# Kernel tuning notes

Hardware: AMD Instinct MI355X
Metric: run time of the kernel (lower is better)

Reference implementation:

```python
import jax, jax.numpy as jnp
import numpy as np
import math

B, C, L = 16, 2048, 64

def setup_inputs() -> dict:
    key = jax.random.key(0)
    kq, kk, kv = jax.random.split(key, 3)
    q = jax.random.normal(kq, (B, C, L), dtype=jnp.float32)
    k = jax.random.normal(kk, (B, C, L), dtype=jnp.float32)
    v = jax.random.normal(kv, (B, C, L), dtype=jnp.float32)
    return {"q": q, "k": k, "v": v}

def reference(q, k, v):
    b, c, l = q.shape
    # Faithful to the torch source: k is RESHAPED (row-major), not transposed.
    k_t = k.reshape(b, l, c)                      # (b, l, c)
    score = jnp.matmul(q, k_t) / math.sqrt(l)     # (b, c, c)
    # nn.Softmax() with no dim on a 3D tensor -> torch implicit dim = 0 (batch axis)
    score = jax.nn.softmax(score, axis=0)
    return jnp.matmul(score, v)                   # (b, c, l)
```

## Files before the change

### kernel.cpp

```cpp
#include <hip/hip_runtime.h>

typedef __attribute__((ext_vector_type(8))) short short8;
typedef __attribute__((ext_vector_type(4))) float float4v;

#define BATCH 16
#define CDIM 2048
#define LDIM 64
#define BSTRIDE (CDIM * LDIM)

__device__ __forceinline__ float bf2f(unsigned short u) {
    return __uint_as_float(((unsigned int)u) << 16);
}
__device__ __forceinline__ unsigned short f2bf(float f) {
    unsigned int x = __float_as_uint(f);
    x += 0x7fffu + ((x >> 16) & 1u);
    return (unsigned short)(x >> 16);
}
__device__ __forceinline__ void dma16(const void* g, void* l) {
    __builtin_amdgcn_global_load_lds(
        (const __attribute__((address_space(1))) void*)g,
        (__attribute__((address_space(3))) void*)l, 16, 0, 0);
}

__global__ __launch_bounds__(256) void prepass_kernel(
    const float* __restrict__ q, const float* __restrict__ k, const float* __restrict__ v,
    unsigned short* __restrict__ qb,
    unsigned short* __restrict__ kT, unsigned short* __restrict__ vS)
{
    __shared__ unsigned short T[64][68];
    const int bx = blockIdx.x;
    const int t = threadIdx.x;

    if (bx < 1024) {
        int i = bx * 256 + t;
        const float4v* src = (const float4v*)q + (size_t)i * 2;
        float4v x0 = src[0], x1 = src[1];
        unsigned int u0 = f2bf(x0[0] * 0.125f) | ((unsigned)f2bf(x0[1] * 0.125f) << 16);
        unsigned int u1 = f2bf(x0[2] * 0.125f) | ((unsigned)f2bf(x0[3] * 0.125f) << 16);
        unsigned int u2 = f2bf(x1[0] * 0.125f) | ((unsigned)f2bf(x1[1] * 0.125f) << 16);
        unsigned int u3 = f2bf(x1[2] * 0.125f) | ((unsigned)f2bf(x1[3] * 0.125f) << 16);
        int b = i >> 14, r = i & 16383, m = r >> 3, j = r & 7;
        *(uint4*)(qb + (size_t)b * BSTRIDE + m * 64 + (j ^ (m & 7)) * 8) =
            make_uint4(u0, u1, u2, u3);
    } else if (bx < 1536) {
        int idx = bx - 1024, b = idx >> 5, n0 = (idx & 31) * 64;
        const float* src = k + (size_t)b * BSTRIDE + (size_t)(t >> 2) * 2048 + n0 + (t & 3) * 16;
#pragma unroll
        for (int kk = 0; kk < 4; kk++) {
            float4v x = *(const float4v*)(src + kk * 4);
#pragma unroll
            for (int e = 0; e < 4; e++)
                T[t >> 2][(t & 3) * 16 + kk * 4 + e] = f2bf(x[e]);
        }
        __syncthreads();
        unsigned short* dst = kT + (size_t)b * BSTRIDE;
        int n = t & 63;
#pragma unroll
        for (int jj = 0; jj < 2; jj++) {
            int j = (t >> 6) * 2 + jj;
            ushort4 g0, g1;
#pragma unroll
            for (int e = 0; e < 4; e++) { g0[e] = T[j * 8 + e][n]; g1[e] = T[j * 8 + 4 + e][n]; }
            *(uint4*)(dst + (size_t)(n0 + n) * 64 + (j ^ (n & 7)) * 8) =
                make_uint4(g0.x | ((unsigned)g0.y << 16), g0.z | ((unsigned)g0.w << 16),
                           g1.x | ((unsigned)g1.y << 16), g1.z | ((unsigned)g1.w << 16));
        }
    } else {
        int idx = bx - 1536, b = idx >> 5, n0 = (idx & 31) * 64;
        const float* src = v + (size_t)b * BSTRIDE + (size_t)n0 * 64 +
                           (size_t)(t >> 2) * 64 + (t & 3) * 16;
#pragma unroll
        for (int kk = 0; kk < 4; kk++) {
            float4v x = *(const float4v*)(src + kk * 4);
#pragma unroll
            for (int e = 0; e < 4; e++)
                T[t >> 2][(t & 3) * 16 + kk * 4 + e] = f2bf(x[e]);
        }
        __syncthreads();
        unsigned short* dst = vS + (size_t)b * BSTRIDE;
        int j = t & 63, qc = t >> 6;
#pragma unroll
        for (int nb = 0; nb < 2; nb++) {
            ushort4 g0, g1;
#pragma unroll
            for (int e = 0; e < 4; e++) {
                g0[e] = T[nb * 32 + qc * 8 + e][j];
                g1[e] = T[nb * 32 + qc * 8 + 4 + e][j];
            }
            *(uint4*)(dst + (size_t)(n0 / 32 + nb) * 2048 + j * 32 + (qc ^ (j & 3)) * 8) =
                make_uint4(g0.x | ((unsigned)g0.y << 16), g0.z | ((unsigned)g0.w << 16),
                           g1.x | ((unsigned)g1.y << 16), g1.z | ((unsigned)g1.w << 16));
        }
    }
}

__global__ __launch_bounds__(256, 2) void dinv_kernel(
    const unsigned short* __restrict__ qb, const unsigned short* __restrict__ kT,
    unsigned short* __restrict__ Dt)
{
    __shared__ unsigned short Sq[2][8192];
    __shared__ unsigned short Sk[2][4096];
    const int tid = threadIdx.x, w = tid >> 6, lane = tid & 63;
    const int c = lane & 15, q = lane >> 4;
    const int mt = blockIdx.x & 15, ng = blockIdx.x >> 4;
    const int m0 = mt * 128, n0 = ng * 64;

    float4v Dacc[2][4];
#pragma unroll
    for (int ms = 0; ms < 2; ms++)
#pragma unroll
        for (int nt = 0; nt < 4; nt++) Dacc[ms][nt] = (float4v){0.f, 0.f, 0.f, 0.f};

    {
        const char* qg = (const char*)(qb + (size_t)m0 * 64);
        const char* kg = (const char*)(kT + (size_t)n0 * 64);
#pragma unroll
        for (int kk = 0; kk < 4; kk++)
            dma16(qg + (w * 4 + kk) * 1024 + lane * 16, (char*)Sq[0] + (w * 4 + kk) * 1024);
        dma16(kg + (w * 2 + 0) * 1024 + lane * 16, (char*)Sk[0] + (w * 2 + 0) * 1024);
        dma16(kg + (w * 2 + 1) * 1024 + lane * 16, (char*)Sk[0] + (w * 2 + 1) * 1024);
    }

    for (int bb = 0; bb < BATCH; bb++) {
        const int p = bb & 1;
        if (bb < BATCH - 1) {
            const char* qg = (const char*)(qb + (size_t)(bb + 1) * BSTRIDE + (size_t)m0 * 64);
            const char* kg = (const char*)(kT + (size_t)(bb + 1) * BSTRIDE + (size_t)n0 * 64);
#pragma unroll
            for (int kk = 0; kk < 4; kk++)
                dma16(qg + (w * 4 + kk) * 1024 + lane * 16, (char*)Sq[p ^ 1] + (w * 4 + kk) * 1024);
            dma16(kg + (w * 2 + 0) * 1024 + lane * 16, (char*)Sk[p ^ 1] + (w * 2 + 0) * 1024);
            dma16(kg + (w * 2 + 1) * 1024 + lane * 16, (char*)Sk[p ^ 1] + (w * 2 + 1) * 1024);
            asm volatile("s_waitcnt vmcnt(6)" ::: "memory");
        } else {
            asm volatile("s_waitcnt vmcnt(0)" ::: "memory");
        }
        asm volatile("s_barrier" ::: "memory");

        short8 Qf[2][2];
#pragma unroll
        for (int ms = 0; ms < 2; ms++)
#pragma unroll
            for (int h = 0; h < 2; h++)
                Qf[ms][h] = *(const short8*)&Sq[p][(w * 32 + ms * 16 + c) * 64 +
                                                  ((h * 4 + q) ^ (c & 7)) * 8];
#pragma unroll
        for (int nt = 0; nt < 4; nt++) {
            short8 A0 = *(const short8*)&Sk[p][(nt * 16 + c) * 64 + (q ^ (c & 7)) * 8];
            short8 A1 = *(const short8*)&Sk[p][(nt * 16 + c) * 64 + ((4 + q) ^ (c & 7)) * 8];
#pragma unroll
            for (int ms = 0; ms < 2; ms++) {
                float4v d = (float4v){0.f, 0.f, 0.f, 0.f};
                d = __builtin_amdgcn_mfma_f32_16x16x32_bf16(A0, Qf[ms][0], d, 0, 0, 0);
                d = __builtin_amdgcn_mfma_f32_16x16x32_bf16(A1, Qf[ms][1], d, 0, 0, 0);
#pragma unroll
                for (int r = 0; r < 4; r++) Dacc[ms][nt][r] += __expf(d[r]);
            }
        }
        asm volatile("s_barrier" ::: "memory");
    }

#pragma unroll
    for (int ms = 0; ms < 2; ms++)
#pragma unroll
        for (int nt = 0; nt < 4; nt++) {
            unsigned int x = f2bf(1.f / Dacc[ms][nt][0]) |
                             ((unsigned)f2bf(1.f / Dacc[ms][nt][1]) << 16);
            unsigned int y = f2bf(1.f / Dacc[ms][nt][2]) |
                             ((unsigned)f2bf(1.f / Dacc[ms][nt][3]) << 16);
            size_t T = (size_t)(mt * 64 + ng * 2 + (nt >> 1));
            *(uint2*)((char*)Dt + T * 8192 + w * 2048 + (ms * 2 + (nt & 1)) * 512 + lane * 8) =
                make_uint2(x, y);
        }
}

__global__ __launch_bounds__(1024, 4) void attn_main_kernel(
    const unsigned short* __restrict__ qb, const unsigned short* __restrict__ kT,
    const unsigned short* __restrict__ vS, const unsigned short* __restrict__ Dt,
    float* __restrict__ out)
{
    __shared__ unsigned short Sk[4][2][2048];
    __shared__ unsigned short Sv[4][2][2048];
    __shared__ unsigned short Ep[16][2][16][40];

    const int tid = threadIdx.x, w = tid >> 6, lane = tid & 63;
    const int c = lane & 15, q = lane >> 4;
    const int g = w >> 2, ns = w & 3;
    const int b = blockIdx.x & 15, mt = blockIdx.x >> 4;
    const int m0 = mt * 128 + g * 32;
    const int nbase = ns * 512;

    const unsigned short* qb_b = qb + (size_t)b * BSTRIDE;
    const char* kbase = (const char*)(kT + (size_t)b * BSTRIDE);
    const char* vbase = (const char*)(vS + (size_t)b * BSTRIDE);

    short8 Qf[2][2];
#pragma unroll
    for (int ms = 0; ms < 2; ms++)
#pragma unroll
        for (int h = 0; h < 2; h++)
            Qf[ms][h] = *(const short8*)(qb_b + (m0 + ms * 16 + c) * 64 +
                                         ((h * 4 + q) ^ (c & 7)) * 8);
    float4v acc[2][4];
#pragma unroll
    for (int ms = 0; ms < 2; ms++)
#pragma unroll
        for (int jt = 0; jt < 4; jt++) acc[ms][jt] = (float4v){0.f, 0.f, 0.f, 0.f};

    dma16(kbase + (size_t)nbase * 128 + g * 1024 + lane * 16, (char*)Sk[ns][0] + g * 1024);
    dma16(vbase + (size_t)(ns * 16) * 4096 + g * 1024 + lane * 16, (char*)Sv[ns][0] + g * 1024);

    for (int st = 0; st < 16; st++) {
        const int p = st & 1;
        if (st < 15) {
            const int n1 = nbase + (st + 1) * 32;
            dma16(kbase + (size_t)n1 * 128 + g * 1024 + lane * 16, (char*)Sk[ns][p ^ 1] + g * 1024);
            dma16(vbase + (size_t)(ns * 16 + st + 1) * 4096 + g * 1024 + lane * 16,
                  (char*)Sv[ns][p ^ 1] + g * 1024);
            asm volatile("s_waitcnt vmcnt(2)" ::: "memory");
        } else {
            asm volatile("s_waitcnt vmcnt(0)" ::: "memory");
        }
        asm volatile("s_barrier" ::: "memory");

        const char* dtb = (const char*)Dt + (size_t)(mt * 64 + ns * 16 + st) * 8192 +
                          g * 2048 + lane * 8;
        uint2 du[2][2];
        du[0][0] = *(const uint2*)(dtb + 0);
        du[0][1] = *(const uint2*)(dtb + 512);
        du[1][0] = *(const uint2*)(dtb + 1024);
        du[1][1] = *(const uint2*)(dtb + 1536);

#pragma unroll
        for (int nt = 0; nt < 2; nt++) {
            short8 A0 = *(const short8*)&Sk[ns][p][(nt * 16 + c) * 64 + (q ^ (c & 7)) * 8];
            short8 A1 = *(const short8*)&Sk[ns][p][(nt * 16 + c) * 64 + ((4 + q) ^ (c & 7)) * 8];
#pragma unroll
            for (int ms = 0; ms < 2; ms++) {
                float4v d = (float4v){0.f, 0.f, 0.f, 0.f};
                d = __builtin_amdgcn_mfma_f32_16x16x32_bf16(A0, Qf[ms][0], d, 0, 0, 0);
                d = __builtin_amdgcn_mfma_f32_16x16x32_bf16(A1, Qf[ms][1], d, 0, 0, 0);
                uint2 u2 = du[ms][nt];
                ushort4 e;
                e.x = f2bf(__expf(d[0]) * __uint_as_float(u2.x << 16));
                e.y = f2bf(__expf(d[1]) * __uint_as_float(u2.x & 0xffff0000u));
                e.z = f2bf(__expf(d[2]) * __uint_as_float(u2.y << 16));
                e.w = f2bf(__expf(d[3]) * __uint_as_float(u2.y & 0xffff0000u));
                *(ushort4*)&Ep[w][ms][c][nt * 16 + q * 4] = e;
            }
        }
        asm volatile("s_waitcnt lgkmcnt(0)" ::: "memory");

        short8 Vf[4];
#pragma unroll
        for (int jt = 0; jt < 4; jt++)
            Vf[jt] = *(const short8*)&Sv[ns][p][(jt * 16 + c) * 32 + (q ^ (c & 3)) * 8];
#pragma unroll
        for (int ms = 0; ms < 2; ms++) {
            short8 Pf = *(const short8*)&Ep[w][ms][c][q * 8];
#pragma unroll
            for (int jt = 0; jt < 4; jt++)
                acc[ms][jt] = __builtin_amdgcn_mfma_f32_16x16x32_bf16(Pf, Vf[jt], acc[ms][jt], 0, 0, 0);
        }
        asm volatile("s_barrier" ::: "memory");
    }

    float* Racc = (float*)&Sk[0][0][0];
    float* Rg = Racc + g * 2176;
    __syncthreads();
#pragma unroll 1
    for (int round = 0; round < 4; round++) {
        if (ns == round) {
#pragma unroll
            for (int ms = 0; ms < 2; ms++)
#pragma unroll
                for (int jt = 0; jt < 4; jt++)
#pragma unroll
                    for (int r = 0; r < 4; r++) {
                        int idx = (ms * 16 + q * 4 + r) * 68 + jt * 16 + c;
                        if (round == 0) Rg[idx] = acc[ms][jt][r];
                        else Rg[idx] += acc[ms][jt][r];
                    }
        }
        __syncthreads();
    }
    {
        int mrow = tid >> 3, col0 = (tid & 7) * 8;
        const float* src = Racc + (mrow >> 5) * 2176 + (mrow & 31) * 68 + col0;
        float4v v0 = *(const float4v*)(src);
        float4v v1 = *(const float4v*)(src + 4);
        float* dst = out + ((size_t)b * CDIM + mt * 128 + mrow) * LDIM + col0;
        *(float4v*)(dst) = v0;
        *(float4v*)(dst + 4) = v1;
    }
}

extern "C" void kernel_launch(void* const* d_in, const int* in_sizes, int n_in,
                              void* d_out, int out_size, void* d_ws, size_t ws_size,
                              hipStream_t stream) {
    const float* q = (const float*)d_in[0];
    const float* k = (const float*)d_in[1];
    const float* v = (const float*)d_in[2];
    float* out = (float*)d_out;

    unsigned short* qb = (unsigned short*)d_ws;
    unsigned short* kT = qb + (size_t)BATCH * BSTRIDE;
    unsigned short* vS = kT + (size_t)BATCH * BSTRIDE;
    unsigned short* Dt = vS + (size_t)BATCH * BSTRIDE;

    prepass_kernel<<<2048, 256, 0, stream>>>(q, k, v, qb, kT, vS);
    dinv_kernel<<<512, 256, 0, stream>>>(qb, kT, Dt);
    attn_main_kernel<<<256, 1024, 0, stream>>>(qb, kT, vS, Dt, out);
}
```

Before: 129.6 us.

## Use exp2 with folded scale, register-shuffle P, smaller main blocks, new Dt layout

Folds log2(e) into the q pre-scale so the kernels can call the hardware exp2 builtin, and uses the rcp builtin for the denominators. The main kernel moves from 1024-thread to 512-thread blocks over 64-row tiles. It builds the P operand with lane shuffles instead of an LDS round trip, prefetches the denominator tiles one step ahead in a coalesced layout, and replaces the four-round reduction with a two-stage one. The dinv kernel gets a flat shared buffer, a higher occupancy hint and a single wait-and-barrier per iteration. This adds a matching swizzle change in V and risks more register pressure and shuffle cost.

```diff
diff --git a/kernel.cpp b/kernel.cpp
--- a/kernel.cpp
+++ b/kernel.cpp
@@ -7,6 +7,14 @@
 #define CDIM 2048
 #define LDIM 64
 #define BSTRIDE (CDIM * LDIM)
+
+#if __has_builtin(__builtin_amdgcn_exp2f)
+#define EXPW(x) __builtin_amdgcn_exp2f(x)
+#define QSCALE 0.18033688011112042f
+#else
+#define EXPW(x) __expf(x)
+#define QSCALE 0.125f
+#endif
 
 __device__ __forceinline__ float bf2f(unsigned short u) {
     return __uint_as_float(((unsigned int)u) << 16);
@@ -35,10 +43,10 @@
         int i = bx * 256 + t;
         const float4v* src = (const float4v*)q + (size_t)i * 2;
         float4v x0 = src[0], x1 = src[1];
-        unsigned int u0 = f2bf(x0[0] * 0.125f) | ((unsigned)f2bf(x0[1] * 0.125f) << 16);
-        unsigned int u1 = f2bf(x0[2] * 0.125f) | ((unsigned)f2bf(x0[3] * 0.125f) << 16);
-        unsigned int u2 = f2bf(x1[0] * 0.125f) | ((unsigned)f2bf(x1[1] * 0.125f) << 16);
-        unsigned int u3 = f2bf(x1[2] * 0.125f) | ((unsigned)f2bf(x1[3] * 0.125f) << 16);
+        unsigned int u0 = f2bf(x0[0] * QSCALE) | ((unsigned)f2bf(x0[1] * QSCALE) << 16);
+        unsigned int u1 = f2bf(x0[2] * QSCALE) | ((unsigned)f2bf(x0[3] * QSCALE) << 16);
+        unsigned int u2 = f2bf(x1[0] * QSCALE) | ((unsigned)f2bf(x1[1] * QSCALE) << 16);
+        unsigned int u3 = f2bf(x1[2] * QSCALE) | ((unsigned)f2bf(x1[3] * QSCALE) << 16);
         int b = i >> 14, r = i & 16383, m = r >> 3, j = r & 7;
         *(uint4*)(qb + (size_t)b * BSTRIDE + m * 64 + (j ^ (m & 7)) * 8) =
             make_uint4(u0, u1, u2, u3);
@@ -79,6 +87,7 @@
         __syncthreads();
         unsigned short* dst = vS + (size_t)b * BSTRIDE;
         int j = t & 63, qc = t >> 6;
+        int sw = qc ^ (j & 3) ^ ((j >> 2) & 3);
 #pragma unroll
         for (int nb = 0; nb < 2; nb++) {
             ushort4 g0, g1;
@@ -87,23 +96,23 @@
                 g0[e] = T[nb * 32 + qc * 8 + e][j];
                 g1[e] = T[nb * 32 + qc * 8 + 4 + e][j];
             }
-            *(uint4*)(dst + (size_t)(n0 / 32 + nb) * 2048 + j * 32 + (qc ^ (j & 3)) * 8) =
+            *(uint4*)(dst + (size_t)(n0 / 32 + nb) * 2048 + j * 32 + sw * 8) =
                 make_uint4(g0.x | ((unsigned)g0.y << 16), g0.z | ((unsigned)g0.w << 16),
                            g1.x | ((unsigned)g1.y << 16), g1.z | ((unsigned)g1.w << 16));
         }
     }
 }
 
-__global__ __launch_bounds__(256, 2) void dinv_kernel(
+__global__ __launch_bounds__(256, 3) void dinv_kernel(
     const unsigned short* __restrict__ qb, const unsigned short* __restrict__ kT,
     unsigned short* __restrict__ Dt)
 {
-    __shared__ unsigned short Sq[2][8192];
-    __shared__ unsigned short Sk[2][4096];
+    __shared__ __align__(16) unsigned char smem[49152];
+
     const int tid = threadIdx.x, w = tid >> 6, lane = tid & 63;
     const int c = lane & 15, q = lane >> 4;
-    const int mt = blockIdx.x & 15, ng = blockIdx.x >> 4;
-    const int m0 = mt * 128, n0 = ng * 64;
+    const int mtB = blockIdx.x & 15, ng = blockIdx.x >> 4;
+    const int m0 = mtB * 128, n0 = ng * 64;
 
     float4v Dacc[2][4];
 #pragma unroll
@@ -116,90 +125,92 @@
         const char* kg = (const char*)(kT + (size_t)n0 * 64);
 #pragma unroll
         for (int kk = 0; kk < 4; kk++)
-            dma16(qg + (w * 4 + kk) * 1024 + lane * 16, (char*)Sq[0] + (w * 4 + kk) * 1024);
-        dma16(kg + (w * 2 + 0) * 1024 + lane * 16, (char*)Sk[0] + (w * 2 + 0) * 1024);
-        dma16(kg + (w * 2 + 1) * 1024 + lane * 16, (char*)Sk[0] + (w * 2 + 1) * 1024);
+            dma16(qg + (w * 4 + kk) * 1024 + lane * 16, (char*)smem + (w * 4 + kk) * 1024);
+        dma16(kg + (w * 2 + 0) * 1024 + lane * 16, (char*)smem + 32768 + (w * 2 + 0) * 1024);
+        dma16(kg + (w * 2 + 1) * 1024 + lane * 16, (char*)smem + 32768 + (w * 2 + 1) * 1024);
     }
 
     for (int bb = 0; bb < BATCH; bb++) {
         const int p = bb & 1;
+        asm volatile("s_waitcnt vmcnt(0)" ::: "memory");
+        asm volatile("s_barrier" ::: "memory");
         if (bb < BATCH - 1) {
             const char* qg = (const char*)(qb + (size_t)(bb + 1) * BSTRIDE + (size_t)m0 * 64);
             const char* kg = (const char*)(kT + (size_t)(bb + 1) * BSTRIDE + (size_t)n0 * 64);
 #pragma unroll
             for (int kk = 0; kk < 4; kk++)
-                dma16(qg + (w * 4 + kk) * 1024 + lane * 16, (char*)Sq[p ^ 1] + (w * 4 + kk) * 1024);
-            dma16(kg + (w * 2 + 0) * 1024 + lane * 16, (char*)Sk[p ^ 1] + (w * 2 + 0) * 1024);
-            dma16(kg + (w * 2 + 1) * 1024 + lane * 16, (char*)Sk[p ^ 1] + (w * 2 + 1) * 1024);
-            asm volatile("s_waitcnt vmcnt(6)" ::: "memory");
-        } else {
-            asm volatile("s_waitcnt vmcnt(0)" ::: "memory");
-        }
-        asm volatile("s_barrier" ::: "memory");
-
+                dma16(qg + (w * 4 + kk) * 1024 + lane * 16,
+                      (char*)smem + (p ^ 1) * 16384 + (w * 4 + kk) * 1024);
+            dma16(kg + (w * 2 + 0) * 1024 + lane * 16,
+                  (char*)smem + 32768 + (p ^ 1) * 8192 + (w * 2 + 0) * 1024);
+            dma16(kg + (w * 2 + 1) * 1024 + lane * 16,
+                  (char*)smem + 32768 + (p ^ 1) * 8192 + (w * 2 + 1) * 1024);
+        }
+        const char* sq = (const char*)smem + p * 16384;
+        const char* sk = (const char*)smem + 32768 + p * 8192;
         short8 Qf[2][2];
 #pragma unroll
         for (int ms = 0; ms < 2; ms++)
 #pragma unroll
             for (int h = 0; h < 2; h++)
-                Qf[ms][h] = *(const short8*)&Sq[p][(w * 32 + ms * 16 + c) * 64 +
-                                                  ((h * 4 + q) ^ (c & 7)) * 8];
+                Qf[ms][h] = *(const short8*)(sq + (w * 32 + ms * 16 + c) * 128 +
+                                             ((h * 4 + q) ^ (c & 7)) * 16);
 #pragma unroll
         for (int nt = 0; nt < 4; nt++) {
-            short8 A0 = *(const short8*)&Sk[p][(nt * 16 + c) * 64 + (q ^ (c & 7)) * 8];
-            short8 A1 = *(const short8*)&Sk[p][(nt * 16 + c) * 64 + ((4 + q) ^ (c & 7)) * 8];
+            short8 A0 = *(const short8*)(sk + (nt * 16 + c) * 128 + ((q) ^ (c & 7)) * 16);
+            short8 A1 = *(const short8*)(sk + (nt * 16 + c) * 128 + ((4 + q) ^ (c & 7)) * 16);
 #pragma unroll
             for (int ms = 0; ms < 2; ms++) {
                 float4v d = (float4v){0.f, 0.f, 0.f, 0.f};
                 d = __builtin_amdgcn_mfma_f32_16x16x32_bf16(A0, Qf[ms][0], d, 0, 0, 0);
                 d = __builtin_amdgcn_mfma_f32_16x16x32_bf16(A1, Qf[ms][1], d, 0, 0, 0);
 #pragma unroll
-                for (int r = 0; r < 4; r++) Dacc[ms][nt][r] += __expf(d[r]);
+                for (int r = 0; r < 4; r++) Dacc[ms][nt][r] += EXPW(d[r]);
             }
         }
-        asm volatile("s_barrier" ::: "memory");
     }
 
 #pragma unroll
     for (int ms = 0; ms < 2; ms++)
 #pragma unroll
         for (int nt = 0; nt < 4; nt++) {
-            unsigned int x = f2bf(1.f / Dacc[ms][nt][0]) |
-                             ((unsigned)f2bf(1.f / Dacc[ms][nt][1]) << 16);
-            unsigned int y = f2bf(1.f / Dacc[ms][nt][2]) |
-                             ((unsigned)f2bf(1.f / Dacc[ms][nt][3]) << 16);
-            size_t T = (size_t)(mt * 64 + ng * 2 + (nt >> 1));
-            *(uint2*)((char*)Dt + T * 8192 + w * 2048 + (ms * 2 + (nt & 1)) * 512 + lane * 8) =
+            unsigned int x = f2bf(__builtin_amdgcn_rcpf(Dacc[ms][nt][0])) |
+                             ((unsigned)f2bf(__builtin_amdgcn_rcpf(Dacc[ms][nt][1])) << 16);
+            unsigned int y = f2bf(__builtin_amdgcn_rcpf(Dacc[ms][nt][2])) |
+                             ((unsigned)f2bf(__builtin_amdgcn_rcpf(Dacc[ms][nt][3])) << 16);
+            size_t tm = (size_t)(mtB * 8 + w * 2 + ms);
+            size_t tp = (size_t)(ng * 2 + (nt >> 1));
+            *(uint2*)((char*)Dt + (tm * 64 + tp) * 1024 + c * 64 + q * 16 + (nt & 1) * 8) =
                 make_uint2(x, y);
         }
 }
 
-__global__ __launch_bounds__(1024, 4) void attn_main_kernel(
+__global__ __launch_bounds__(512, 4) void attn_main_kernel(
     const unsigned short* __restrict__ qb, const unsigned short* __restrict__ kT,
     const unsigned short* __restrict__ vS, const unsigned short* __restrict__ Dt,
     float* __restrict__ out)
 {
-    __shared__ unsigned short Sk[4][2][2048];
-    __shared__ unsigned short Sv[4][2][2048];
-    __shared__ unsigned short Ep[16][2][16][40];
+    __shared__ __align__(16) unsigned char smem[65536];
 
     const int tid = threadIdx.x, w = tid >> 6, lane = tid & 63;
     const int c = lane & 15, q = lane >> 4;
     const int g = w >> 2, ns = w & 3;
     const int b = blockIdx.x & 15, mt = blockIdx.x >> 4;
-    const int m0 = mt * 128 + g * 32;
+    const int m0 = mt * 64;
     const int nbase = ns * 512;
 
     const unsigned short* qb_b = qb + (size_t)b * BSTRIDE;
     const char* kbase = (const char*)(kT + (size_t)b * BSTRIDE);
     const char* vbase = (const char*)(vS + (size_t)b * BSTRIDE);
+    char* skb = (char*)smem + ns * 8192;
+    char* svb = (char*)smem + 32768 + ns * 8192;
 
     short8 Qf[2][2];
 #pragma unroll
     for (int ms = 0; ms < 2; ms++)
 #pragma unroll
         for (int h = 0; h < 2; h++)
-            Qf[ms][h] = *(const short8*)(qb_b + (m0 + ms * 16 + c) * 64 +
+            Qf[ms][h] = *(const short8*)(qb_b + (m0 + g * 32 + ms * 16 + c) * 64 +
                                          ((h * 4 + q) ^ (c & 7)) * 8);
     float4v acc[2][4];
 #pragma unroll
@@ -207,91 +218,120 @@
 #pragma unroll
         for (int jt = 0; jt < 4; jt++) acc[ms][jt] = (float4v){0.f, 0.f, 0.f, 0.f};
 
-    dma16(kbase + (size_t)nbase * 128 + g * 1024 + lane * 16, (char*)Sk[ns][0] + g * 1024);
-    dma16(vbase + (size_t)(ns * 16) * 4096 + g * 1024 + lane * 16, (char*)Sv[ns][0] + g * 1024);
+    const char* dtw0 = (const char*)Dt +
+        ((size_t)(mt * 4 + g * 2 + 0) * 64 + ns * 16) * 1024 + c * 64 + q * 16;
+    const char* dtw1 = dtw0 + (size_t)64 * 1024;
+
+    dma16(kbase + (size_t)nbase * 128 + (2 * g + 0) * 1024 + lane * 16, skb + (2 * g + 0) * 1024);
+    dma16(kbase + (size_t)nbase * 128 + (2 * g + 1) * 1024 + lane * 16, skb + (2 * g + 1) * 1024);
+    dma16(vbase + (size_t)(ns * 16) * 4096 + (2 * g + 0) * 1024 + lane * 16, svb + (2 * g + 0) * 1024);
+    dma16(vbase + (size_t)(ns * 16) * 4096 + (2 * g + 1) * 1024 + lane * 16, svb + (2 * g + 1) * 1024);
+    uint4 du[2];
+    du[0] = *(const uint4*)(dtw0);
+    du[1] = *(const uint4*)(dtw1);
 
     for (int st = 0; st < 16; st++) {
         const int p = st & 1;
+        asm volatile("s_waitcnt vmcnt(0)" ::: "memory");
+        asm volatile("s_barrier" ::: "memory");
+
+        uint4 nu[2] = {du[0], du[1]};
         if (st < 15) {
             const int n1 = nbase + (st + 1) * 32;
-            dma16(kbase + (size_t)n1 * 128 + g * 1024 + lane * 16, (char*)Sk[ns][p ^ 1] + g * 1024);
-            dma16(vbase + (size_t)(ns * 16 + st + 1) * 4096 + g * 1024 + lane * 16,
-                  (char*)Sv[ns][p ^ 1] + g * 1024);
-            asm volatile("s_waitcnt vmcnt(2)" ::: "memory");
-        } else {
-            asm volatile("s_waitcnt vmcnt(0)" ::: "memory");
-        }
-        asm volatile("s_barrier" ::: "memory");
-
-        const char* dtb = (const char*)Dt + (size_t)(mt * 64 + ns * 16 + st) * 8192 +
-                          g * 2048 + lane * 8;
-        uint2 du[2][2];
-        du[0][0] = *(const uint2*)(dtb + 0);
-        du[0][1] = *(const uint2*)(dtb + 512);
-        du[1][0] = *(const uint2*)(dtb + 1024);
-        du[1][1] = *(const uint2*)(dtb + 1536);
-
+            dma16(kbase + (size_t)n1 * 128 + (2 * g + 0) * 1024 + lane * 16,
+                  skb + (p ^ 1) * 4096 + (2 * g + 0) * 1024);
+            dma16(kbase + (size_t)n1 * 128 + (2 * g + 1) * 1024 + lane * 16,
+                  skb + (p ^ 1) * 4096 + (2 * g + 1) * 1024);
+            dma16(vbase + (size_t)(ns * 16 + st + 1) * 4096 + (2 * g + 0) * 1024 + lane * 16,
+                  svb + (p ^ 1) * 4096 + (2 * g + 0) * 1024);
+            dma16(vbase + (size_t)(ns * 16 + st + 1) * 4096 + (2 * g + 1) * 1024 + lane * 16,
+                  svb + (p ^ 1) * 4096 + (2 * g + 1) * 1024);
+            nu[0] = *(const uint4*)(dtw0 + (size_t)(st + 1) * 1024);
+            nu[1] = *(const uint4*)(dtw1 + (size_t)(st + 1) * 1024);
+        }
+
+        const char* skp = skb + p * 4096;
+        unsigned int pr[2][2][2];
 #pragma unroll
         for (int nt = 0; nt < 2; nt++) {
-            short8 A0 = *(const short8*)&Sk[ns][p][(nt * 16 + c) * 64 + (q ^ (c & 7)) * 8];
-            short8 A1 = *(const short8*)&Sk[ns][p][(nt * 16 + c) * 64 + ((4 + q) ^ (c & 7)) * 8];
+            short8 A0 = *(const short8*)(skp + (nt * 16 + c) * 128 + ((q) ^ (c & 7)) * 16);
+            short8 A1 = *(const short8*)(skp + (nt * 16 + c) * 128 + ((4 + q) ^ (c & 7)) * 16);
 #pragma unroll
             for (int ms = 0; ms < 2; ms++) {
                 float4v d = (float4v){0.f, 0.f, 0.f, 0.f};
                 d = __builtin_amdgcn_mfma_f32_16x16x32_bf16(A0, Qf[ms][0], d, 0, 0, 0);
                 d = __builtin_amdgcn_mfma_f32_16x16x32_bf16(A1, Qf[ms][1], d, 0, 0, 0);
-                uint2 u2 = du[ms][nt];
-                ushort4 e;
-                e.x = f2bf(__expf(d[0]) * __uint_as_float(u2.x << 16));
-                e.y = f2bf(__expf(d[1]) * __uint_as_float(u2.x & 0xffff0000u));
-                e.z = f2bf(__expf(d[2]) * __uint_as_float(u2.y << 16));
-                e.w = f2bf(__expf(d[3]) * __uint_as_float(u2.y & 0xffff0000u));
-                *(ushort4*)&Ep[w][ms][c][nt * 16 + q * 4] = e;
+                unsigned int ux = nt ? du[ms].z : du[ms].x;
+                unsigned int uy = nt ? du[ms].w : du[ms].y;
+                float p0 = EXPW(d[0]) * __uint_as_float(ux << 16);
+                float p1 = EXPW(d[1]) * __uint_as_float(ux & 0xffff0000u);
+                float p2 = EXPW(d[2]) * __uint_as_float(uy << 16);
+                float p3 = EXPW(d[3]) * __uint_as_float(uy & 0xffff0000u);
+                pr[ms][nt][0] = f2bf(p0) | ((unsigned)f2bf(p1) << 16);
+                pr[ms][nt][1] = f2bf(p2) | ((unsigned)f2bf(p3) << 16);
             }
         }
-        asm volatile("s_waitcnt lgkmcnt(0)" ::: "memory");
-
-        short8 Vf[4];
-#pragma unroll
-        for (int jt = 0; jt < 4; jt++)
-            Vf[jt] = *(const short8*)&Sv[ns][p][(jt * 16 + c) * 32 + (q ^ (c & 3)) * 8];
-#pragma unroll
-        for (int ms = 0; ms < 2; ms++) {
-            short8 Pf = *(const short8*)&Ep[w][ms][c][q * 8];
-#pragma unroll
-            for (int jt = 0; jt < 4; jt++)
-                acc[ms][jt] = __builtin_amdgcn_mfma_f32_16x16x32_bf16(Pf, Vf[jt], acc[ms][jt], 0, 0, 0);
-        }
-        asm volatile("s_barrier" ::: "memory");
-    }
-
-    float* Racc = (float*)&Sk[0][0][0];
-    float* Rg = Racc + g * 2176;
+
+        union PU { unsigned int i[4]; short8 s; };
+        PU pu0, pu1;
+#pragma unroll
+        for (int t = 0; t < 4; t++) {
+            int src = (2 * (q & 1) + (t >> 1)) * 16 + c;
+            int a0 = __shfl((int)pr[0][0][t & 1], src);
+            int b0 = __shfl((int)pr[0][1][t & 1], src);
+            pu0.i[t] = (unsigned int)((q >= 2) ? b0 : a0);
+            int a1 = __shfl((int)pr[1][0][t & 1], src);
+            int b1 = __shfl((int)pr[1][1][t & 1], src);
+            pu1.i[t] = (unsigned int)((q >= 2) ? b1 : a1);
+        }
+
+        const char* svp = svb + p * 4096;
+#pragma unroll
+        for (int jt = 0; jt < 4; jt++) {
+            short8 Vf = *(const short8*)(svp + (jt * 16 + c) * 64 +
+                                         ((q ^ (c & 3) ^ ((c >> 2) & 3))) * 16);
+            acc[0][jt] = __builtin_amdgcn_mfma_f32_16x16x32_bf16(pu0.s, Vf, acc[0][jt], 0, 0, 0);
+            acc[1][jt] = __builtin_amdgcn_mfma_f32_16x16x32_bf16(pu1.s, Vf, acc[1][jt], 0, 0, 0);
+        }
+        du[0] = nu[0]; du[1] = nu[1];
+    }
+
     __syncthreads();
-#pragma unroll 1
-    for (int round = 0; round < 4; round++) {
-        if (ns == round) {
+    {
+        float* cpy = (float*)((char*)smem + (ns & 1) * 17408);
+        if (ns < 2) {
 #pragma unroll
             for (int ms = 0; ms < 2; ms++)
 #pragma unroll
                 for (int jt = 0; jt < 4; jt++)
 #pragma unroll
-                    for (int r = 0; r < 4; r++) {
-                        int idx = (ms * 16 + q * 4 + r) * 68 + jt * 16 + c;
-                        if (round == 0) Rg[idx] = acc[ms][jt][r];
-                        else Rg[idx] += acc[ms][jt][r];
-                    }
-        }
-        __syncthreads();
-    }
+                    for (int r = 0; r < 4; r++)
+                        cpy[(g * 32 + ms * 16 + q * 4 + r) * 68 + jt * 16 + c] = acc[ms][jt][r];
+        }
+    }
+    __syncthreads();
     {
-        int mrow = tid >> 3, col0 = (tid & 7) * 8;
-        const float* src = Racc + (mrow >> 5) * 2176 + (mrow & 31) * 68 + col0;
-        float4v v0 = *(const float4v*)(src);
-        float4v v1 = *(const float4v*)(src + 4);
-        float* dst = out + ((size_t)b * CDIM + mt * 128 + mrow) * LDIM + col0;
-        *(float4v*)(dst) = v0;
-        *(float4v*)(dst + 4) = v1;
+        float* cpy = (float*)((char*)smem + (ns & 1) * 17408);
+        if (ns >= 2) {
+#pragma unroll
+            for (int ms = 0; ms < 2; ms++)
+#pragma unroll
+                for (int jt = 0; jt < 4; jt++)
+#pragma unroll
+                    for (int r = 0; r < 4; r++)
+                        cpy[(g * 32 + ms * 16 + q * 4 + r) * 68 + jt * 16 + c] += acc[ms][jt][r];
+        }
+    }
+    __syncthreads();
+    {
+        int ml = tid >> 3, j0 = (tid & 7) * 8;
+        const float* c0 = (const float*)smem + ml * 68 + j0;
+        const float* c1 = (const float*)((char*)smem + 17408) + ml * 68 + j0;
+        float4v s0 = *(const float4v*)c0 + *(const float4v*)c1;
+        float4v s1 = *(const float4v*)(c0 + 4) + *(const float4v*)(c1 + 4);
+        float* dst = out + ((size_t)b * CDIM + m0 + ml) * LDIM + j0;
+        *(float4v*)dst = s0;
+        *(float4v*)(dst + 4) = s1;
     }
 }
 
@@ -310,5 +350,5 @@
 
     prepass_kernel<<<2048, 256, 0, stream>>>(q, k, v, qb, kT, vS);
     dinv_kernel<<<512, 256, 0, stream>>>(qb, kT, Dt);
-    attn_main_kernel<<<256, 1024, 0, stream>>>(qb, kT, vS, Dt, out);
-}
+    attn_main_kernel<<<512, 512, 0, stream>>>(qb, kT, vS, Dt, out);
+}
```

Measured after the change: 126.6 us. -2.3%, faster.
